# Kernel tuning notes

Hardware: AMD Instinct MI355X
Metric: run time of the kernel (lower is better)

Reference implementation:

```python
import jax, jax.numpy as jnp
import numpy as np

H = 16  # num_heads
DH = 64  # head_dim
HID = 1024
NEG_INF = float('-inf')


def _rotate_half(x):
    d = x.shape[-1]
    x1 = x[..., : d // 2]
    x2 = x[..., d // 2 : (d // 2) * 2]
    return jnp.concatenate([-x2, x1], axis=-1)


def _rope_cos_sin(L, D):
    inv_freq = 1.0 / (10000.0 ** (jnp.arange(0, D, 2, dtype=jnp.float32) / D))
    t = jnp.arange(L, dtype=jnp.float32)
    freqs = t[:, None] * inv_freq[None, :]            # (L, D/2)
    cos = jnp.repeat(jnp.cos(freqs), 2, axis=-1)[:, :D]
    sin = jnp.repeat(jnp.sin(freqs), 2, axis=-1)[:, :D]
    return cos[None, None], sin[None, None]           # (1,1,L,D)


def setup_inputs() -> dict:
    key = jax.random.key(0)
    ks = jax.random.split(key, 24)
    B, L, D = 2, 2048, HID
    s = 0.02
    inp = {
        'query': jax.random.normal(ks[0], (B, L, D), jnp.float32),
        'key': jax.random.normal(ks[1], (B, L, D), jnp.float32),
        'value': jax.random.normal(ks[2], (B, L, D), jnp.float32),
        'attn_mask': jnp.ones((B, L, L), dtype=bool),
        'action_ids': jax.random.randint(ks[3], (B, L), 0, 3, jnp.int32),
        'time_deltas': jax.random.randint(ks[4], (B, L), 0, 128, jnp.int32),
        'Wq': jax.random.normal(ks[5], (D, D), jnp.float32) * s,
        'bq': jnp.zeros((D,), jnp.float32),
        'Wk': jax.random.normal(ks[6], (D, D), jnp.float32) * s,
        'bk': jnp.zeros((D,), jnp.float32),
        'Wv': jax.random.normal(ks[7], (D, D), jnp.float32) * s,
        'bv': jnp.zeros((D,), jnp.float32),
        'Wu': jax.random.normal(ks[8], (D, D), jnp.float32) * s,
        'bu': jnp.zeros((D,), jnp.float32),
        'Wo': jax.random.normal(ks[9], (D, D), jnp.float32) * s,
        'bo': jnp.zeros((D,), jnp.float32),
        'action_emb': jax.random.normal(ks[10], (3, 16), jnp.float32).at[0].set(0.0),
        'Wap': jax.random.normal(ks[11], (16, D), jnp.float32) * s,
        'bap': jnp.zeros((D,), jnp.float32),
        'td_emb': (jax.random.normal(ks[12], (128, H), jnp.float32) * 0.1).at[0].set(0.0),
        'td_gate': jnp.float32(0.0),
    }
    return inp


def reference(query, key, value, attn_mask, action_ids, time_deltas,
              Wq, bq, Wk, bk, Wv, bv, Wu, bu, Wo, bo,
              action_emb, Wap, bap, td_emb, td_gate):
    B, L, D = query.shape
    Q = query @ Wq + bq
    K = key @ Wk + bk
    V = value @ Wv + bv
    U = query @ Wu + bu
    # sigmoid action gate added to U before gating V
    g = action_emb[action_ids] @ Wap + bap            # (B,L,D)
    U = U + g
    def split(x):
        return x.reshape(B, L, H, DH).transpose(0, 2, 1, 3)  # (B,H,L,Dh)
    Q, K, V, U = split(Q), split(K), split(V), split(U)
    V = V * jax.nn.sigmoid(U)
    # inline RoPE
    cos, sin = _rope_cos_sin(L, DH)
    Q = Q * cos + _rotate_half(Q) * sin
    K = K * cos + _rotate_half(K) * sin
    # learned time-delta additive bias over key positions
    td = jnp.clip(time_deltas.astype(jnp.int32), 0, td_emb.shape[0] - 1)
    bias = td_emb[td]                                  # (B,L,H)
    bias = bias.transpose(0, 2, 1)[:, :, None, :]      # (B,H,1,L)
    mask_float = jnp.where(attn_mask[:, None], 0.0, NEG_INF).astype(Q.dtype)
    mask_float = mask_float + jax.nn.sigmoid(td_gate) * bias
    scale = DH ** -0.5
    scores = jnp.einsum('bhqd,bhkd->bhqk', Q, K) * scale + mask_float
    attn = jax.nn.softmax(scores, axis=-1)
    out = jnp.einsum('bhqk,bhkd->bhqd', attn, V)       # (B,H,L,Dh)
    out = out.transpose(0, 2, 1, 3).reshape(B, L, D)
    return out @ Wo + bo
```

## Files before the change

kernel.cpp:

```cpp
#include <hip/hip_runtime.h>
#include <hip/hip_bf16.h>
#include <math.h>


using bf16 = __hip_bfloat16;
typedef __bf16 bf16x8 __attribute__((ext_vector_type(8)));
typedef __bf16 bf16x4 __attribute__((ext_vector_type(4)));
typedef float f32x4 __attribute__((ext_vector_type(4)));

#define LSEQ 2048
#define MROWS 4096
#define DMODEL 1024
#define NCHUNK 2
#define CHUNKLEN (LSEQ / NCHUNK)
#define NT (CHUNKLEN / 64)

__device__ inline f32x4 mfma16(bf16x8 a, bf16x8 b, f32x4 c) {
    return __builtin_amdgcn_mfma_f32_16x16x32_bf16(a, b, c, 0, 0, 0);
}

__device__ inline void gload_lds16(const __bf16* g, __bf16* l) {
    __builtin_amdgcn_global_load_lds(
        (const __attribute__((address_space(1))) unsigned int*)(unsigned long long)(const void*)g,
        (__attribute__((address_space(3))) unsigned int*)(unsigned int)(unsigned long long)(void*)l,
        16, 0, 0);
}

__global__ __launch_bounds__(256) void transpose5(const float* __restrict__ W0,
                                                  const float* __restrict__ W1,
                                                  const float* __restrict__ W2,
                                                  const float* __restrict__ W3,
                                                  const float* __restrict__ W4,
                                                  __bf16* __restrict__ WtBase) {
    int z = blockIdx.z;
    const float* W = z == 0 ? W0 : z == 1 ? W1 : z == 2 ? W2 : z == 3 ? W3 : W4;
    __bf16* Wt = WtBase + (size_t)z * DMODEL * DMODEL;
    __shared__ __bf16 t[64][65];
    int bx = blockIdx.x * 64, by = blockIdx.y * 64;
    int tx = threadIdx.x & 63, ty0 = threadIdx.x >> 6;
    for (int ty = ty0; ty < 64; ty += 4)
        t[ty][tx] = (__bf16)W[(size_t)(by + ty) * DMODEL + bx + tx];
    __syncthreads();
    for (int ty = ty0; ty < 64; ty += 4)
        Wt[(size_t)(bx + ty) * DMODEL + by + tx] = t[tx][ty];
}

__global__ __launch_bounds__(256) void cast3(const float* __restrict__ q,
                                             const float* __restrict__ k,
                                             const float* __restrict__ v,
                                             __bf16* __restrict__ qc,
                                             __bf16* __restrict__ kc,
                                             __bf16* __restrict__ vc) {
    size_t i = ((size_t)blockIdx.x * 256 + threadIdx.x) * 8;
    f32x4 a0 = *(const f32x4*)(q + i), a1 = *(const f32x4*)(q + i + 4);
    f32x4 b0 = *(const f32x4*)(k + i), b1 = *(const f32x4*)(k + i + 4);
    f32x4 c0 = *(const f32x4*)(v + i), c1 = *(const f32x4*)(v + i + 4);
    bf16x8 ra, rb, rc;
#pragma unroll
    for (int j = 0; j < 4; ++j) {
        ra[j] = (__bf16)a0[j]; ra[4 + j] = (__bf16)a1[j];
        rb[j] = (__bf16)b0[j]; rb[4 + j] = (__bf16)b1[j];
        rc[j] = (__bf16)c0[j]; rc[4 + j] = (__bf16)c1[j];
    }
    *(bf16x8*)(qc + i) = ra;
    *(bf16x8*)(kc + i) = rb;
    *(bf16x8*)(vc + i) = rc;
}

__global__ __launch_bounds__(256) void prep(const float* __restrict__ action_emb,
                                            const float* __restrict__ Wap,
                                            const float* __restrict__ bap,
                                            const float* __restrict__ td_emb,
                                            const float* __restrict__ td_gate,
                                            const int* __restrict__ time_deltas,
                                            float* __restrict__ gtable,
                                            float* __restrict__ biasT) {
    int i = blockIdx.x * 256 + threadIdx.x;
    if (i < 3 * DMODEL) {
        int a = i >> 10, n = i & 1023;
        float s = bap[n];
        for (int j = 0; j < 16; ++j)
            s += action_emb[a * 16 + j] * Wap[j * DMODEL + n];
        gtable[i] = s;
    }
    if (i < 2 * 16 * LSEQ) {
        float gate = 1.f / (1.f + __expf(-td_gate[0]));
        int b = i >> 15, h = (i >> 11) & 15, key = i & 2047;
        int td = time_deltas[b * LSEQ + key];
        td = td < 0 ? 0 : (td > 127 ? 127 : td);
        biasT[i] = gate * td_emb[td * 16 + h] * 1.4426950408889634f
                   - 5.7707801635558534f;
    }
}

__global__ __launch_bounds__(256, 4) void proj_gemm(
        const __bf16* __restrict__ Qc, const __bf16* __restrict__ Kc,
        const __bf16* __restrict__ Vc, const __bf16* __restrict__ Wt4,
        const float* __restrict__ bq, const float* __restrict__ bk,
        const float* __restrict__ bv, const float* __restrict__ bu,
        const float* __restrict__ gtable, const int* __restrict__ action_ids,
        __bf16* __restrict__ XhBase) {
    int id = blockIdx.x + 64 * (blockIdx.y + 8 * blockIdx.z);
    int sid = (id & 7) * 256 + (id >> 3);
    int m0 = (sid & 63) * 64;
    int n0 = ((sid >> 6) & 7) * 128;
    int sel = sid >> 9;

    const __bf16* A = (sel == 1) ? Kc : (sel == 2 ? Vc : Qc);
    const __bf16* Bn = Wt4 + (size_t)sel * DMODEL * DMODEL;
    const float* bvec = sel == 0 ? bq : sel == 1 ? bk : (sel == 2 ? bv : bu);
    __bf16* out = XhBase + (size_t)sel * MROWS * DMODEL;

    __shared__ __align__(16) __bf16 As[64 * 64];
    __shared__ __align__(16) __bf16 Bs[128 * 64];
    int tid = threadIdx.x;
    int lane = tid & 63, w = tid >> 6;
    int l15 = lane & 15, quad = lane >> 4;
    int wm = w >> 1, wn = w & 1;

    int rA = tid >> 3, sA = tid & 7;
    int xsl = (sA ^ (rA & 7)) * 8;
    const __bf16* AgT = A  + (size_t)(m0 + rA) * DMODEL + xsl;
    const __bf16* BgT = Bn + (size_t)(n0 + rA) * DMODEL + xsl;
    __bf16* AsD = As + tid * 8;
    __bf16* BsD = Bs + tid * 8;

    int x7 = l15 & 7;
    int e0 = ((0 + quad) ^ x7) * 8;
    int e1 = ((4 + quad) ^ x7) * 8;

    f32x4 acc[2][4] = {};
    for (int k0 = 0; k0 < DMODEL; k0 += 64) {
        __syncthreads();
        gload_lds16(AgT + k0, AsD);
        gload_lds16(AgT + (size_t)32 * DMODEL + k0, AsD + 2048);
        gload_lds16(BgT + k0, BsD);
        gload_lds16(BgT + (size_t)32 * DMODEL + k0, BsD + 2048);
        gload_lds16(BgT + (size_t)64 * DMODEL + k0, BsD + 4096);
        gload_lds16(BgT + (size_t)96 * DMODEL + k0, BsD + 6144);
        __syncthreads();
        bf16x8 af[2][2], bfr[4][2];
        const __bf16* ap = As + (wm * 32 + l15) * 64;
        const __bf16* bp = Bs + (wn * 64 + l15) * 64;
#pragma unroll
        for (int s = 0; s < 2; ++s) {
            af[s][0] = *(const bf16x8*)(ap + s * 16 * 64 + e0);
            af[s][1] = *(const bf16x8*)(ap + s * 16 * 64 + e1);
        }
#pragma unroll
        for (int s = 0; s < 4; ++s) {
            bfr[s][0] = *(const bf16x8*)(bp + s * 16 * 64 + e0);
            bfr[s][1] = *(const bf16x8*)(bp + s * 16 * 64 + e1);
        }
#pragma unroll
        for (int sm = 0; sm < 2; ++sm)
#pragma unroll
            for (int sn = 0; sn < 4; ++sn) {
                acc[sm][sn] = mfma16(af[sm][0], bfr[sn][0], acc[sm][sn]);
                acc[sm][sn] = mfma16(af[sm][1], bfr[sn][1], acc[sm][sn]);
            }
    }
#pragma unroll
    for (int sn = 0; sn < 4; ++sn) {
        int n = n0 + wn * 64 + sn * 16 + l15;
        float bb = bvec[n];
        int hh = n >> 6, dh = n & 63;
#pragma unroll
        for (int sm = 0; sm < 2; ++sm)
#pragma unroll
            for (int r = 0; r < 4; ++r) {
                int row = m0 + wm * 32 + sm * 16 + quad * 4 + r;
                float v = acc[sm][sn][r] + bb;
                if (sel == 3) v += gtable[action_ids[row] * DMODEL + n];
                int b = row >> 11, l = row & 2047;
                out[((size_t)(b * 16 + hh) * LSEQ + l) * 64 + dh] = (__bf16)v;
            }
    }
}

__global__ __launch_bounds__(256) void rope_gate(__bf16* __restrict__ Qh,
                                                 __bf16* __restrict__ Kh,
                                                 const __bf16* __restrict__ Vh,
                                                 const __bf16* __restrict__ Uh,
                                                 __bf16* __restrict__ Vt) {
    int bh = blockIdx.y;
    int lt = blockIdx.x * 64;
    const float C = 0.4152410118609203f;
    const float QSC = 0.18033688011112043f;
    int tid = threadIdx.x;

    {
        int l = tid >> 2, jp = tid & 3;
        float pos = (float)(lt + l);
        float c1[4], s1[4], c2[4], s2[4];
#pragma unroll
        for (int u = 0; u < 4; ++u) {
            int d2 = jp * 4 + u;
            __sincosf(pos * exp2f(-(float)d2 * C), &s1[u], &c1[u]);
            __sincosf(pos * exp2f(-(float)(16 + d2) * C), &s2[u], &c2[u]);
        }
        size_t base = ((size_t)bh * LSEQ + lt + l) * 64 + jp * 8;
        bf16x8 qlo = *(bf16x8*)(Qh + base), qhi = *(bf16x8*)(Qh + base + 32);
        bf16x8 klo = *(bf16x8*)(Kh + base), khi = *(bf16x8*)(Kh + base + 32);
        bf16x8 oql, oqh, okl, okh;
#pragma unroll
        for (int t = 0; t < 8; ++t) {
            int u = t >> 1;
            float ql = (float)qlo[t], qh = (float)qhi[t];
            oql[t] = (__bf16)((ql * c1[u] - qh * s1[u]) * QSC);
            oqh[t] = (__bf16)((qh * c2[u] + ql * s2[u]) * QSC);
            float kl = (float)klo[t], kh = (float)khi[t];
            okl[t] = (__bf16)(kl * c1[u] - kh * s1[u]);
            okh[t] = (__bf16)(kh * c2[u] + kl * s2[u]);
        }
        *(bf16x8*)(Qh + base) = oql; *(bf16x8*)(Qh + base + 32) = oqh;
        *(bf16x8*)(Kh + base) = okl; *(bf16x8*)(Kh + base + 32) = okh;
    }

    __shared__ __bf16 tile[64][65];
    const __bf16* Vb = Vh + ((size_t)bh * LSEQ + lt) * 64;
    const __bf16* Ub = Uh + ((size_t)bh * LSEQ + lt) * 64;
#pragma unroll
    for (int it = 0; it < 2; ++it) {
        int idx = it * 256 + tid;
        int r = idx >> 3, c = (idx & 7) * 8;
        bf16x8 v = *(const bf16x8*)(Vb + (size_t)r * 64 + c);
        bf16x8 u = *(const bf16x8*)(Ub + (size_t)r * 64 + c);
#pragma unroll
        for (int t = 0; t < 8; ++t)
            tile[r][c + t] = (__bf16)((float)v[t] / (1.f + __expf(-(float)u[t])));
    }
    __syncthreads();
    __bf16* Vtb = Vt + (size_t)bh * 64 * LSEQ + lt;
#pragma unroll
    for (int it = 0; it < 2; ++it) {
        int idx = it * 256 + tid;
        int dh = idx >> 3, lc = (idx & 7) * 8;
        bf16x8 o;
#pragma unroll
        for (int t = 0; t < 8; ++t) o[t] = tile[lc + t][dh];
        *(bf16x8*)(Vtb + (size_t)dh * LSEQ + lc) = o;
    }
}

__global__ __launch_bounds__(256, 5) void flash_attn(
        const __bf16* __restrict__ Qh, const __bf16* __restrict__ Kh,
        const __bf16* __restrict__ Vt, const float* __restrict__ biasT,
        float* __restrict__ opart0, float* __restrict__ opart1,
        float* __restrict__ lsumB) {
    __shared__ __align__(16) __bf16 Ks[2][64 * 64];
    __shared__ __align__(16) __bf16 Vs[64 * 64];
    __shared__ __align__(16) __bf16 pP[4][16][64];

    int id = blockIdx.x + 32 * blockIdx.y + 1024 * blockIdx.z;
    int sid = (id & 7) * 256 + (id >> 3);
    int qt = (sid & 31) * 64;
    int bh = (sid >> 5) & 31;
    int ck = sid >> 10;

    int tid = threadIdx.x;
    int lane = tid & 63, w = tid >> 6;
    int l15 = lane & 15, quad = lane >> 4;

    const __bf16* Qb = Qh + (size_t)bh * LSEQ * 64;
    const __bf16* Kb = Kh + (size_t)bh * LSEQ * 64;
    const __bf16* Vb = Vt + (size_t)bh * 64 * LSEQ;
    const float* bT = biasT + (size_t)bh * LSEQ;

    int q0 = qt + w * 16;
    bf16x8 aQ0 = *(const bf16x8*)(Qb + (size_t)(q0 + l15) * 64 + quad * 8);
    bf16x8 aQ1 = *(const bf16x8*)(Qb + (size_t)(q0 + l15) * 64 + 32 + quad * 8);

    int iA = tid, iB = tid + 256;
    int rA = iA >> 3, xA = ((iA & 7) ^ (rA & 7)) * 8;
    int rB = iB >> 3, xB = ((iB & 7) ^ (rB & 7)) * 8;
    const __bf16* kgA = Kb + (size_t)rA * 64 + xA;
    const __bf16* kgB = Kb + (size_t)rB * 64 + xB;
    const __bf16* vgA = Vb + (size_t)rA * LSEQ + xA;
    const __bf16* vgB = Vb + (size_t)rB * LSEQ + xB;

    int x7 = l15 & 7;
    int eh0 = l15 * 64 + ((quad)     ^ x7) * 8;
    int eh1 = l15 * 64 + ((4 + quad) ^ x7) * 8;

    __bf16* pw = &pP[w][l15][0];
    int wof0 = ((0 + quad) ^ l15) << 2;
    int wof1 = ((4 + quad) ^ l15) << 2;
    int wof2 = ((8 + quad) ^ l15) << 2;
    int wof3 = ((12 + quad) ^ l15) << 2;
    int rof0a = ((2 * quad) ^ l15) << 2;
    int rof0b = ((2 * quad + 1) ^ l15) << 2;
    int rof1a = ((8 + 2 * quad) ^ l15) << 2;
    int rof1b = ((9 + 2 * quad) ^ l15) << 2;

    int kbeg = ck * CHUNKLEN;
    gload_lds16(kgA + (size_t)kbeg * 64, &Ks[0][w * 512]);
    gload_lds16(kgB + (size_t)kbeg * 64, &Ks[0][2048 + w * 512]);
    __syncthreads();

    f32x4 o[4] = {};
    float lsum = 0.f;

#pragma unroll 2
    for (int t = 0; t < NT; ++t) {
        int kt = kbeg + t * 64;
        int cb = t & 1, nb = cb ^ 1;
        f32x4 bias4[4];
#pragma unroll
        for (int s = 0; s < 4; ++s)
            bias4[s] = *(const f32x4*)(bT + kt + s * 16 + quad * 4);
        gload_lds16(vgA + kt, &Vs[w * 512]);
        gload_lds16(vgB + kt, &Vs[2048 + w * 512]);
        if (t + 1 < NT) {
            gload_lds16(kgA + (size_t)(kt + 64) * 64, &Ks[nb][w * 512]);
            gload_lds16(kgB + (size_t)(kt + 64) * 64, &Ks[nb][2048 + w * 512]);
        }
        const __bf16* kp = &Ks[cb][0];
        float rs = 0.f;
        int wofs[4] = {wof0, wof1, wof2, wof3};
#pragma unroll
        for (int s = 0; s < 4; ++s) {
            bf16x8 k0 = *(const bf16x8*)(kp + eh0 + s * 1024);
            bf16x8 k1 = *(const bf16x8*)(kp + eh1 + s * 1024);
            f32x4 st = bias4[s];
            __builtin_amdgcn_s_setprio(1);
            st = mfma16(k0, aQ0, st);
            st = mfma16(k1, aQ1, st);
            __builtin_amdgcn_s_setprio(0);
            bf16x4 pk;
#pragma unroll
            for (int r = 0; r < 4; ++r) {
                float e = exp2f(st[r]);
                rs += e;
                pk[r] = (__bf16)e;
            }
            *(bf16x4*)(pw + wofs[s]) = pk;
        }
        rs += __shfl_xor(rs, 16);
        rs += __shfl_xor(rs, 32);
        lsum += rs;
        asm volatile("s_waitcnt lgkmcnt(0)" ::: "memory");
        union { bf16x8 v8; bf16x4 v4[2]; } u0, u1;
        u0.v4[0] = *(const bf16x4*)(pw + rof0a);
        u0.v4[1] = *(const bf16x4*)(pw + rof0b);
        u1.v4[0] = *(const bf16x4*)(pw + rof1a);
        u1.v4[1] = *(const bf16x4*)(pw + rof1b);
        bf16x8 aP0 = u0.v8, aP1 = u1.v8;
        __syncthreads();
        const __bf16* vp = &Vs[0];
        __builtin_amdgcn_s_setprio(1);
#pragma unroll
        for (int s = 0; s < 4; ++s) {
            bf16x8 v0 = *(const bf16x8*)(vp + eh0 + s * 1024);
            bf16x8 v1 = *(const bf16x8*)(vp + eh1 + s * 1024);
            o[s] = mfma16(aP0, v0, o[s]);
            o[s] = mfma16(aP1, v1, o[s]);
        }
        __builtin_amdgcn_s_setprio(0);
        __syncthreads();
    }
    if (lane < 16)
        lsumB[((size_t)ck * 32 + bh) * LSEQ + q0 + lane] = lsum;
    float* op = (ck ? opart1 : opart0) + ((size_t)bh * LSEQ + q0) * 64;
#pragma unroll
    for (int r = 0; r < 4; ++r) {
#pragma unroll
        for (int s = 0; s < 4; ++s)
            op[(size_t)(quad * 4 + r) * 64 + s * 16 + l15] = o[s][r];
    }
}

__global__ __launch_bounds__(256) void reduce_norm(const float* __restrict__ op0,
                                                   const float* __restrict__ op1,
                                                   const float* __restrict__ lsumB,
                                                   __bf16* __restrict__ Oh) {
    size_t i = (size_t)blockIdx.x * 256 + threadIdx.x;
    size_t row = i >> 3;
    int dp = ((int)i & 7) * 8;
    f32x4 a0 = *(const f32x4*)(op0 + row * 64 + dp);
    f32x4 a1 = *(const f32x4*)(op0 + row * 64 + dp + 4);
    f32x4 b0 = *(const f32x4*)(op1 + row * 64 + dp);
    f32x4 b1 = *(const f32x4*)(op1 + row * 64 + dp + 4);
    float inv = 1.f / (lsumB[row] + lsumB[row + (size_t)32 * LSEQ]);
    bf16x8 rv;
#pragma unroll
    for (int j = 0; j < 4; ++j) {
        rv[j]     = (__bf16)((a0[j] + b0[j]) * inv);
        rv[4 + j] = (__bf16)((a1[j] + b1[j]) * inv);
    }
    int bh = (int)(row >> 11), q = (int)row & 2047;
    int b = bh >> 4, h = bh & 15;
    *(bf16x8*)(Oh + ((size_t)(b * 2048 + q) * DMODEL) + h * 64 + dp) = rv;
}

__global__ __launch_bounds__(256, 4) void out_gemm(const __bf16* __restrict__ Oh,
                                                   const __bf16* __restrict__ WtO,
                                                   const float* __restrict__ bo,
                                                   float* __restrict__ outp) {
    int id = blockIdx.x + 64 * blockIdx.y;
    int sid = (id & 7) * 128 + (id >> 3);
    int m0 = (sid & 63) * 64;
    int n0 = (sid >> 6) * 64;

    __shared__ __align__(16) __bf16 As[64 * 64];
    __shared__ __align__(16) __bf16 Bs[64 * 64];
    int tid = threadIdx.x;
    int lane = tid & 63, w = tid >> 6;
    int l15 = lane & 15, quad = lane >> 4;
    int wm = w >> 1, wn = w & 1;

    int rA = tid >> 3, sA = tid & 7;
    int xsl = (sA ^ (rA & 7)) * 8;
    const __bf16* Ag = Oh  + (size_t)(m0 + rA) * DMODEL + xsl;
    const __bf16* Bg = WtO + (size_t)(n0 + rA) * DMODEL + xsl;
    __bf16* AsD = As + tid * 8;
    __bf16* BsD = Bs + tid * 8;

    int x7 = l15 & 7;
    int e0 = ((0 + quad) ^ x7) * 8;
    int e1 = ((4 + quad) ^ x7) * 8;

    f32x4 acc[2][2] = {};
    for (int k0 = 0; k0 < DMODEL; k0 += 64) {
        __syncthreads();
        gload_lds16(Ag + k0, AsD);
        gload_lds16(Ag + (size_t)32 * DMODEL + k0, AsD + 2048);
        gload_lds16(Bg + k0, BsD);
        gload_lds16(Bg + (size_t)32 * DMODEL + k0, BsD + 2048);
        __syncthreads();
        bf16x8 af[2][2], bfr[2][2];
        const __bf16* ap = As + (wm * 32 + l15) * 64;
        const __bf16* bp = Bs + (wn * 32 + l15) * 64;
#pragma unroll
        for (int s = 0; s < 2; ++s) {
            af[s][0]  = *(const bf16x8*)(ap + s * 16 * 64 + e0);
            af[s][1]  = *(const bf16x8*)(ap + s * 16 * 64 + e1);
            bfr[s][0] = *(const bf16x8*)(bp + s * 16 * 64 + e0);
            bfr[s][1] = *(const bf16x8*)(bp + s * 16 * 64 + e1);
        }
#pragma unroll
        for (int sm = 0; sm < 2; ++sm)
#pragma unroll
            for (int sn = 0; sn < 2; ++sn) {
                acc[sm][sn] = mfma16(af[sm][0], bfr[sn][0], acc[sm][sn]);
                acc[sm][sn] = mfma16(af[sm][1], bfr[sn][1], acc[sm][sn]);
            }
    }
#pragma unroll
    for (int sn = 0; sn < 2; ++sn) {
        int n = n0 + wn * 32 + sn * 16 + l15;
        float bb = bo[n];
#pragma unroll
        for (int sm = 0; sm < 2; ++sm)
#pragma unroll
            for (int r = 0; r < 4; ++r) {
                int row = m0 + wm * 32 + sm * 16 + quad * 4 + r;
                outp[(size_t)row * DMODEL + n] = acc[sm][sn][r] + bb;
            }
    }
}

extern "C" void kernel_launch(void* const* d_in, const int* in_sizes, int n_in,
                              void* d_out, int out_size, void* d_ws, size_t ws_size,
                              hipStream_t stream) {
    const float* query = (const float*)d_in[0];
    const float* keyx  = (const float*)d_in[1];
    const float* value = (const float*)d_in[2];
    const int* action_ids  = (const int*)d_in[4];
    const int* time_deltas = (const int*)d_in[5];
    const float* Wq = (const float*)d_in[6];
    const float* bq = (const float*)d_in[7];
    const float* Wk = (const float*)d_in[8];
    const float* bk = (const float*)d_in[9];
    const float* Wv = (const float*)d_in[10];
    const float* bv = (const float*)d_in[11];
    const float* Wu = (const float*)d_in[12];
    const float* bu = (const float*)d_in[13];
    const float* Wo = (const float*)d_in[14];
    const float* bo = (const float*)d_in[15];
    const float* action_emb = (const float*)d_in[16];
    const float* Wap = (const float*)d_in[17];
    const float* bap = (const float*)d_in[18];
    const float* td_emb = (const float*)d_in[19];
    const float* td_gate = (const float*)d_in[20];

    char* w = (char*)d_ws;
    const size_t MB = 1ull << 20;
    const size_t KB = 1024;
    if (ws_size < 59 * MB) return;
    __bf16* Wt4 = (__bf16*)(w + 0 * MB);
    __bf16* WtO = Wt4 + 4ull * DMODEL * DMODEL;
    float* gtable = (float*)(w + 10 * MB);
    float* biasT  = (float*)(w + 10 * MB + 64 * KB);
    __bf16* Qh = (__bf16*)(w + 11 * MB);
    __bf16* Kh = (__bf16*)(w + 19 * MB);
    __bf16* Vh = (__bf16*)(w + 27 * MB);
    __bf16* Uh = (__bf16*)(w + 35 * MB);
    __bf16* Vt = (__bf16*)(w + 0 * MB);
    __bf16* Qc = (__bf16*)(w + 43 * MB);
    __bf16* Kc = (__bf16*)(w + 51 * MB);
    __bf16* Vc = (__bf16*)d_out;
    float* opart0 = (float*)(w + 27 * MB);
    float* opart1 = (float*)(w + 43 * MB);
    float* lsumB  = (float*)((char*)d_out + 8 * MB);
    __bf16* Oh = (__bf16*)(w + 11 * MB);

    transpose5<<<dim3(16, 16, 5), 256, 0, stream>>>(Wq, Wk, Wv, Wu, Wo, Wt4);
    cast3<<<2048, 256, 0, stream>>>(query, keyx, value, Qc, Kc, Vc);
    prep<<<256, 256, 0, stream>>>(action_emb, Wap, bap, td_emb, td_gate,
                                  time_deltas, gtable, biasT);
    proj_gemm<<<dim3(64, 8, 4), 256, 0, stream>>>(Qc, Kc, Vc, Wt4,
                                                  bq, bk, bv, bu,
                                                  gtable, action_ids, Qh);
    rope_gate<<<dim3(32, 32), 256, 0, stream>>>(Qh, Kh, Vh, Uh, Vt);
    flash_attn<<<dim3(32, 32, NCHUNK), 256, 0, stream>>>(Qh, Kh, Vt, biasT,
                                                         opart0, opart1, lsumB);
    reduce_norm<<<2048, 256, 0, stream>>>(opart0, opart1, lsumB, Oh);
    out_gemm<<<dim3(64, 16), 256, 0, stream>>>(Oh, WtO, bo, (float*)d_out);
}
```

Baseline: 343.5 us.

## Relax attention barriers with partial vmcnt waits and revert out_gemm to K=32 tiles

In the attention loop the next K tile is now prefetched unconditionally, and __syncthreads is replaced with explicit s_waitcnt vmcnt counts plus a bare s_barrier, so outstanding global-to-LDS loads are not fully drained at each barrier. The out_gemm kernel moves back to a simpler 32-wide K step with no XOR swizzle and no block-id remapping, which halves LDS use per step but doubles the number of loop iterations and barriers. The unconditional prefetch reads one tile past the chunk end on the last iteration, which may go out of bounds for the final chunk. Fixed vmcnt values depend on the exact number of loads in flight and are fragile.

```diff
diff --git a/kernel.cpp b/kernel.cpp
--- a/kernel.cpp
+++ b/kernel.cpp
@@ -311,10 +311,9 @@
             bias4[s] = *(const f32x4*)(bT + kt + s * 16 + quad * 4);
         gload_lds16(vgA + kt, &Vs[w * 512]);
         gload_lds16(vgB + kt, &Vs[2048 + w * 512]);
-        if (t + 1 < NT) {
-            gload_lds16(kgA + (size_t)(kt + 64) * 64, &Ks[nb][w * 512]);
-            gload_lds16(kgB + (size_t)(kt + 64) * 64, &Ks[nb][2048 + w * 512]);
-        }
+        gload_lds16(kgA + (size_t)(kt + 64) * 64, &Ks[nb][w * 512]);
+        gload_lds16(kgB + (size_t)(kt + 64) * 64, &Ks[nb][2048 + w * 512]);
+        asm volatile("s_waitcnt vmcnt(8)" ::: "memory");
         const __bf16* kp = &Ks[cb][0];
         float rs = 0.f;
         int wofs[4] = {wof0, wof1, wof2, wof3};
@@ -346,7 +345,8 @@
         u1.v4[0] = *(const bf16x4*)(pw + rof1a);
         u1.v4[1] = *(const bf16x4*)(pw + rof1b);
         bf16x8 aP0 = u0.v8, aP1 = u1.v8;
-        __syncthreads();
+        asm volatile("s_waitcnt vmcnt(2)" ::: "memory");
+        __builtin_amdgcn_s_barrier();
         const __bf16* vp = &Vs[0];
         __builtin_amdgcn_s_setprio(1);
 #pragma unroll
@@ -357,7 +357,7 @@
             o[s] = mfma16(aP1, v1, o[s]);
         }
         __builtin_amdgcn_s_setprio(0);
-        __syncthreads();
+        __builtin_amdgcn_s_barrier();
     }
     if (lane < 16)
         lsumB[((size_t)ck * 32 + bh) * LSEQ + q0 + lane] = lsum;
@@ -397,54 +397,39 @@
                                                    const __bf16* __restrict__ WtO,
                                                    const float* __restrict__ bo,
                                                    float* __restrict__ outp) {
-    int id = blockIdx.x + 64 * blockIdx.y;
-    int sid = (id & 7) * 128 + (id >> 3);
-    int m0 = (sid & 63) * 64;
-    int n0 = (sid >> 6) * 64;
-
-    __shared__ __align__(16) __bf16 As[64 * 64];
-    __shared__ __align__(16) __bf16 Bs[64 * 64];
+    __shared__ __align__(16) __bf16 As[64 * 32];
+    __shared__ __align__(16) __bf16 Bs[64 * 32];
     int tid = threadIdx.x;
     int lane = tid & 63, w = tid >> 6;
     int l15 = lane & 15, quad = lane >> 4;
     int wm = w >> 1, wn = w & 1;
-
-    int rA = tid >> 3, sA = tid & 7;
-    int xsl = (sA ^ (rA & 7)) * 8;
-    const __bf16* Ag = Oh  + (size_t)(m0 + rA) * DMODEL + xsl;
-    const __bf16* Bg = WtO + (size_t)(n0 + rA) * DMODEL + xsl;
-    __bf16* AsD = As + tid * 8;
-    __bf16* BsD = Bs + tid * 8;
-
-    int x7 = l15 & 7;
-    int e0 = ((0 + quad) ^ x7) * 8;
-    int e1 = ((4 + quad) ^ x7) * 8;
+    int m0 = blockIdx.x * 64, n0 = blockIdx.y * 64;
+
+    int lr = lane >> 2, lc = (lane & 3) * 8;
+    const __bf16* Ag = Oh  + (size_t)(m0 + w * 16 + lr) * DMODEL + lc;
+    const __bf16* Bg = WtO + (size_t)(n0 + w * 16 + lr) * DMODEL + lc;
+    __bf16* AsW = As + w * 512;
+    __bf16* BsW = Bs + w * 512;
 
     f32x4 acc[2][2] = {};
-    for (int k0 = 0; k0 < DMODEL; k0 += 64) {
+    for (int k0 = 0; k0 < DMODEL; k0 += 32) {
         __syncthreads();
-        gload_lds16(Ag + k0, AsD);
-        gload_lds16(Ag + (size_t)32 * DMODEL + k0, AsD + 2048);
-        gload_lds16(Bg + k0, BsD);
-        gload_lds16(Bg + (size_t)32 * DMODEL + k0, BsD + 2048);
+        gload_lds16(Ag + k0, AsW);
+        gload_lds16(Bg + k0, BsW);
         __syncthreads();
-        bf16x8 af[2][2], bfr[2][2];
-        const __bf16* ap = As + (wm * 32 + l15) * 64;
-        const __bf16* bp = Bs + (wn * 32 + l15) * 64;
+        bf16x8 af[2], bfr[2];
+        const __bf16* ap = As + (wm * 32 + l15) * 32 + quad * 8;
+        const __bf16* bp = Bs + (wn * 32 + l15) * 32 + quad * 8;
 #pragma unroll
         for (int s = 0; s < 2; ++s) {
-            af[s][0]  = *(const bf16x8*)(ap + s * 16 * 64 + e0);
-            af[s][1]  = *(const bf16x8*)(ap + s * 16 * 64 + e1);
-            bfr[s][0] = *(const bf16x8*)(bp + s * 16 * 64 + e0);
-            bfr[s][1] = *(const bf16x8*)(bp + s * 16 * 64 + e1);
+            af[s]  = *(const bf16x8*)(ap + s * 16 * 32);
+            bfr[s] = *(const bf16x8*)(bp + s * 16 * 32);
         }
 #pragma unroll
         for (int sm = 0; sm < 2; ++sm)
 #pragma unroll
-            for (int sn = 0; sn < 2; ++sn) {
-                acc[sm][sn] = mfma16(af[sm][0], bfr[sn][0], acc[sm][sn]);
-                acc[sm][sn] = mfma16(af[sm][1], bfr[sn][1], acc[sm][sn]);
-            }
+            for (int sn = 0; sn < 2; ++sn)
+                acc[sm][sn] = mfma16(af[sm], bfr[sn], acc[sm][sn]);
     }
 #pragma unroll
     for (int sn = 0; sn < 2; ++sn) {
```

Result: no change. 338.7 us (-1.4%).
